# Optimization experiments

Hardware: AMD Instinct MI355X
Metric: run time of the kernel (lower is better)

## Reference

```python
import jax, jax.numpy as jnp
import numpy as np

S = 64   # state_dim
C = 27   # children per internal node


def setup_inputs() -> dict:
    key = jax.random.key(0)
    ks = jax.random.split(key, 16)
    def f(k, shp, scale=0.02):
        return jax.random.normal(k, shp, dtype=jnp.float32) * scale
    return {
        "external_input": f(ks[0], (S, 5), 1.0),
        "state0":  f(ks[1], (S, 5), 0.01),          # root state buffer
        "states1": f(ks[2], (C, S, 5), 0.01),        # 27 level-1 node states
        "states2": f(ks[3], (C, C, S, 5), 0.01),     # 729 leaf states, grouped by parent
        "agg_W0":  f(ks[4], (S * 5, S * 5 * C)),     # root child_aggregator
        "agg_b0":  f(ks[5], (S * 5,)),
        "agg_W1":  f(ks[6], (C, S * 5, S * 5 * C)),  # batched level-1 aggregators
        "agg_b1":  f(ks[7], (C, S * 5)),
        "up_W1_0": f(ks[8], (64, S * 10)),           # root update_net layer 1
        "up_b1_0": f(ks[9], (64,)),
        "up_W2_0": f(ks[10], (S * 5, 64)),           # root update_net layer 2
        "up_b2_0": f(ks[11], (S * 5,)),
        "up_W1_1": f(ks[12], (C, 64, S * 10)),       # batched level-1 update_nets
        "up_b1_1": f(ks[13], (C, 64)),
        "up_W2_1": f(ks[14], (C, S * 5, 64)),
        "up_b2_1": f(ks[15], (C, S * 5)),
    }


def reference(external_input, state0, states1, states2,
              agg_W0, agg_b0, agg_W1, agg_b1,
              up_W1_0, up_b1_0, up_W2_0, up_b2_0,
              up_W1_1, up_b1_1, up_W2_1, up_b2_1):
    # --- level 2 (leaves): forward just returns their state ---
    leaf_flat = states2.reshape(C, C * S * 5)  # per level-1 parent: stacked+flattened children

    # --- level 1: all 27 nodes processed as one batched GEMV ---
    agg1 = jnp.einsum('nij,nj->ni', agg_W1, leaf_flat) + agg_b1        # [27, S*5]
    comb1 = jnp.concatenate([states1.reshape(C, S * 5), agg1], axis=-1)  # [27, S*10]
    h1 = jax.nn.relu(jnp.einsum('nkj,nj->nk', up_W1_1, comb1) + up_b1_1)  # [27, 64]
    upd1 = jnp.einsum('nij,nj->ni', up_W2_1, h1) + up_b2_1             # [27, S*5]
    new_states1 = states1 + upd1.reshape(C, S, 5)

    # --- root: external input added, then aggregate updated children ---
    s0 = state0 + external_input
    agg0 = agg_W0 @ new_states1.reshape(-1) + agg_b0                   # [S*5]
    comb0 = jnp.concatenate([s0.reshape(-1), agg0])                    # [S*10]
    h0 = jax.nn.relu(up_W1_0 @ comb0 + up_b1_0)
    new_state0 = s0 + (up_W2_0 @ h0 + up_b2_0).reshape(S, 5)
    return new_state0
```

## Files before the change

kernel.cpp:

```cpp
#include <hip/hip_runtime.h>
#include <hip/hip_bf16.h>


__device__ __forceinline__ float wave_reduce_sum(float v) {
    v += __shfl_xor(v, 32, 64);
    v += __shfl_xor(v, 16, 64);
    v += __shfl_xor(v, 8, 64);
    v += __shfl_xor(v, 4, 64);
    v += __shfl_xor(v, 2, 64);
    v += __shfl_xor(v, 1, 64);
    return v;
}

__device__ __forceinline__ float fma4s(float4 w, float4 x, float acc) {
    acc = fmaf(w.x, x.x, acc);
    acc = fmaf(w.y, x.y, acc);
    acc = fmaf(w.z, x.z, acc);
    acc = fmaf(w.w, x.w, acc);
    return acc;
}

__device__ __forceinline__ float4 add4(float4 a, float4 b) {
    return make_float4(a.x + b.x, a.y + b.y, a.z + b.z, a.w + b.w);
}

__global__ void __launch_bounds__(256) k1_gemv(
    const float* __restrict__ W,
    const float* __restrict__ x,
    const float* __restrict__ bias,
    float*       __restrict__ y)
{
    const int b    = blockIdx.x;
    const int node = b / 80;
    const int row0 = node * 320 + (b % 80) * 4;
    const int tid  = threadIdx.x;

    const float4* __restrict__ xf  = reinterpret_cast<const float4*>(x) + (size_t)node * 2160;
    const float4* __restrict__ w0p = reinterpret_cast<const float4*>(W) + (size_t)(row0 + 0) * 2160;
    const float4* __restrict__ w1p = reinterpret_cast<const float4*>(W) + (size_t)(row0 + 1) * 2160;
    const float4* __restrict__ w2p = reinterpret_cast<const float4*>(W) + (size_t)(row0 + 2) * 2160;
    const float4* __restrict__ w3p = reinterpret_cast<const float4*>(W) + (size_t)(row0 + 3) * 2160;

    float4 a0 = make_float4(0.f, 0.f, 0.f, 0.f), a1 = a0, a2 = a0, a3 = a0;
    for (int j = tid; j < 2160; j += 256) {
        float4 xv = xf[j];
        float4 w0 = w0p[j];
        float4 w1 = w1p[j];
        float4 w2 = w2p[j];
        float4 w3 = w3p[j];
        a0.x = fmaf(w0.x, xv.x, a0.x); a0.y = fmaf(w0.y, xv.y, a0.y);
        a0.z = fmaf(w0.z, xv.z, a0.z); a0.w = fmaf(w0.w, xv.w, a0.w);
        a1.x = fmaf(w1.x, xv.x, a1.x); a1.y = fmaf(w1.y, xv.y, a1.y);
        a1.z = fmaf(w1.z, xv.z, a1.z); a1.w = fmaf(w1.w, xv.w, a1.w);
        a2.x = fmaf(w2.x, xv.x, a2.x); a2.y = fmaf(w2.y, xv.y, a2.y);
        a2.z = fmaf(w2.z, xv.z, a2.z); a2.w = fmaf(w2.w, xv.w, a2.w);
        a3.x = fmaf(w3.x, xv.x, a3.x); a3.y = fmaf(w3.y, xv.y, a3.y);
        a3.z = fmaf(w3.z, xv.z, a3.z); a3.w = fmaf(w3.w, xv.w, a3.w);
    }
    float s0 = (a0.x + a0.y) + (a0.z + a0.w);
    float s1 = (a1.x + a1.y) + (a1.z + a1.w);
    float s2 = (a2.x + a2.y) + (a2.z + a2.w);
    float s3 = (a3.x + a3.y) + (a3.z + a3.w);
    s0 = wave_reduce_sum(s0);
    s1 = wave_reduce_sum(s1);
    s2 = wave_reduce_sum(s2);
    s3 = wave_reduce_sum(s3);

    __shared__ float red[4][4];
    const int wv = tid >> 6, lane = tid & 63;
    if (lane == 0) { red[wv][0] = s0; red[wv][1] = s1; red[wv][2] = s2; red[wv][3] = s3; }
    __syncthreads();
    if (tid < 4) {
        float v = red[0][tid] + red[1][tid] + red[2][tid] + red[3][tid];
        y[row0 + tid] = v + bias[row0 + tid];
    }
}

__global__ void __launch_bounds__(256) k2a_h(
    const float* __restrict__ states1,
    const float* __restrict__ agg1,
    const float* __restrict__ W1,
    const float* __restrict__ b1,
    float*       __restrict__ h1)
{
    __shared__ float comb[640];
    const int nb  = blockIdx.x;
    const int n   = nb / 16;
    const int tid = threadIdx.x;

    float4* combf = reinterpret_cast<float4*>(comb);
    const float4* __restrict__ s1f = reinterpret_cast<const float4*>(states1) + (size_t)n * 80;
    const float4* __restrict__ a1f = reinterpret_cast<const float4*>(agg1) + (size_t)n * 80;
    if (tid < 80)       combf[tid] = s1f[tid];
    else if (tid < 160) combf[tid] = a1f[tid - 80];
    __syncthreads();

    const int wv = tid >> 6, lane = tid & 63;
    const int k  = (nb % 16) * 4 + wv;
    const float4* __restrict__ Wf = reinterpret_cast<const float4*>(W1) + ((size_t)n * 64 + k) * 160;
    float acc = 0.f;
    #pragma unroll
    for (int j = lane; j < 160; j += 64)
        acc = fma4s(Wf[j], combf[j], acc);
    acc = wave_reduce_sum(acc);
    if (lane == 0) h1[n * 64 + k] = fmaxf(acc + b1[n * 64 + k], 0.f);
}

__global__ void __launch_bounds__(256) k2b_ns(
    const float* __restrict__ states1,
    const float* __restrict__ h1,
    const float* __restrict__ W2,
    const float* __restrict__ b2,
    float*       __restrict__ ns1)
{
    const int tid  = threadIdx.x;
    const int wv   = tid >> 6, lane = tid & 63;
    const int i    = blockIdx.x * 4 + wv;
    const int n    = i / 320;
    float acc = W2[(size_t)i * 64 + lane] * h1[n * 64 + lane];
    acc = wave_reduce_sum(acc);
    if (lane == 0) ns1[i] = states1[i] + acc + b2[i];
}

__global__ void __launch_bounds__(256) k3_gemv(
    const float* __restrict__ W,
    const float* __restrict__ x,
    float*       __restrict__ yp)
{
    const int b   = blockIdx.x;
    const int cs  = b / 80;
    const int r0  = (b % 80) * 4;
    const int tid = threadIdx.x;

    const float4* __restrict__ xf  = reinterpret_cast<const float4*>(x);
    const float4* __restrict__ w0p = reinterpret_cast<const float4*>(W) + (size_t)(r0 + 0) * 2160;
    const float4* __restrict__ w1p = reinterpret_cast<const float4*>(W) + (size_t)(r0 + 1) * 2160;
    const float4* __restrict__ w2p = reinterpret_cast<const float4*>(W) + (size_t)(r0 + 2) * 2160;
    const float4* __restrict__ w3p = reinterpret_cast<const float4*>(W) + (size_t)(r0 + 3) * 2160;

    float4 a0 = make_float4(0.f, 0.f, 0.f, 0.f), a1 = a0, a2 = a0, a3 = a0;
    const int jend = cs * 540 + 540;
    for (int j = cs * 540 + tid; j < jend; j += 256) {
        float4 xv = xf[j];
        float4 w0 = w0p[j];
        float4 w1 = w1p[j];
        float4 w2 = w2p[j];
        float4 w3 = w3p[j];
        a0.x = fmaf(w0.x, xv.x, a0.x); a0.y = fmaf(w0.y, xv.y, a0.y);
        a0.z = fmaf(w0.z, xv.z, a0.z); a0.w = fmaf(w0.w, xv.w, a0.w);
        a1.x = fmaf(w1.x, xv.x, a1.x); a1.y = fmaf(w1.y, xv.y, a1.y);
        a1.z = fmaf(w1.z, xv.z, a1.z); a1.w = fmaf(w1.w, xv.w, a1.w);
        a2.x = fmaf(w2.x, xv.x, a2.x); a2.y = fmaf(w2.y, xv.y, a2.y);
        a2.z = fmaf(w2.z, xv.z, a2.z); a2.w = fmaf(w2.w, xv.w, a2.w);
        a3.x = fmaf(w3.x, xv.x, a3.x); a3.y = fmaf(w3.y, xv.y, a3.y);
        a3.z = fmaf(w3.z, xv.z, a3.z); a3.w = fmaf(w3.w, xv.w, a3.w);
    }
    float s0 = (a0.x + a0.y) + (a0.z + a0.w);
    float s1 = (a1.x + a1.y) + (a1.z + a1.w);
    float s2 = (a2.x + a2.y) + (a2.z + a2.w);
    float s3 = (a3.x + a3.y) + (a3.z + a3.w);
    s0 = wave_reduce_sum(s0);
    s1 = wave_reduce_sum(s1);
    s2 = wave_reduce_sum(s2);
    s3 = wave_reduce_sum(s3);

    __shared__ float red[4][4];
    const int wv = tid >> 6, lane = tid & 63;
    if (lane == 0) { red[wv][0] = s0; red[wv][1] = s1; red[wv][2] = s2; red[wv][3] = s3; }
    __syncthreads();
    if (tid < 4) {
        yp[cs * 320 + r0 + tid] =
            red[0][tid] + red[1][tid] + red[2][tid] + red[3][tid];
    }
}

__global__ void __launch_bounds__(256) K4_root(
    const float* __restrict__ state0,
    const float* __restrict__ ext,
    const float* __restrict__ agg0p,
    const float* __restrict__ aggb0,
    const float* __restrict__ W1,
    const float* __restrict__ b1,
    const float* __restrict__ W2,
    const float* __restrict__ b2,
    float*       __restrict__ out)
{
    __shared__ __align__(16) float comb[640];
    __shared__ float h[64];
    const int tid = threadIdx.x;
    const int wv  = tid >> 6, lane = tid & 63;

    float4* combf = reinterpret_cast<float4*>(comb);
    const float4* __restrict__ s0f = reinterpret_cast<const float4*>(state0);
    const float4* __restrict__ exf = reinterpret_cast<const float4*>(ext);
    const float4* __restrict__ p0  = reinterpret_cast<const float4*>(agg0p);
    const float4* __restrict__ b0f = reinterpret_cast<const float4*>(aggb0);
    if (tid < 80) {
        combf[tid] = add4(s0f[tid], exf[tid]);
    } else if (tid < 160) {
        int jj = tid - 80;
        combf[tid] = add4(add4(add4(p0[jj], p0[80 + jj]), add4(p0[160 + jj], p0[240 + jj])), b0f[jj]);
    }
    __syncthreads();

    const float4* __restrict__ cf = reinterpret_cast<const float4*>(comb);
    for (int kk = 0; kk < 16; ++kk) {
        const int k = wv * 16 + kk;
        const float4* __restrict__ Wf = reinterpret_cast<const float4*>(W1) + (size_t)k * 160;
        float acc = 0.f;
        for (int j = lane; j < 160; j += 64)
            acc = fma4s(Wf[j], cf[j], acc);
        acc = wave_reduce_sum(acc);
        if (lane == 0) h[k] = fmaxf(acc + b1[k], 0.f);
    }
    __syncthreads();

    const int i = blockIdx.x * 4 + wv;
    float acc = W2[(size_t)i * 64 + lane] * h[lane];
    acc = wave_reduce_sum(acc);
    if (lane == 0) out[i] = comb[i] + acc + b2[i];
}

extern "C" void kernel_launch(void* const* d_in, const int* in_sizes, int n_in,
                              void* d_out, int out_size, void* d_ws, size_t ws_size,
                              hipStream_t stream) {
    const float* ext      = (const float*)d_in[0];
    const float* state0   = (const float*)d_in[1];
    const float* states1  = (const float*)d_in[2];
    const float* states2  = (const float*)d_in[3];
    const float* agg_W0   = (const float*)d_in[4];
    const float* agg_b0   = (const float*)d_in[5];
    const float* agg_W1   = (const float*)d_in[6];
    const float* agg_b1   = (const float*)d_in[7];
    const float* up_W1_0  = (const float*)d_in[8];
    const float* up_b1_0  = (const float*)d_in[9];
    const float* up_W2_0  = (const float*)d_in[10];
    const float* up_b2_0  = (const float*)d_in[11];
    const float* up_W1_1  = (const float*)d_in[12];
    const float* up_b1_1  = (const float*)d_in[13];
    const float* up_W2_1  = (const float*)d_in[14];
    const float* up_b2_1  = (const float*)d_in[15];

    float* out   = (float*)d_out;
    float* ws    = (float*)d_ws;
    float* agg1  = ws;
    float* h1    = ws + 8640;
    float* ns1   = ws + 10368;
    float* agg0p = ws + 19008;

    k1_gemv<<<2160, 256, 0, stream>>>(agg_W1, states2, agg_b1, agg1);
    k2a_h  <<<432,  256, 0, stream>>>(states1, agg1, up_W1_1, up_b1_1, h1);
    k2b_ns <<<2160, 256, 0, stream>>>(states1, h1, up_W2_1, up_b2_1, ns1);
    k3_gemv<<<320,  256, 0, stream>>>(agg_W0, ns1, agg0p);
    K4_root<<<80,   256, 0, stream>>>(state0, ext, agg0p, agg_b0,
                                      up_W1_0, up_b1_0, up_W2_0, up_b2_0, out);
}
```

Baseline: 83.29 us.

## Fuse four tail kernels into one launch synchronized by global atomic counters

Merges the h1, new-state, root aggregation and root update stages into a single kernel whose block ranges play each stage role. Dependencies between stages are enforced with per-stage atomic counters that blocks spin on, which removes three kernel launch boundaries and their drain gaps. A memset of the counters is added each call. Spin-waiting relies on producer blocks being scheduled before consumers, and relaxed atomics without fences risk ordering and forward-progress problems. The root aggregation also now reads ns1 as scalar atomic loads rather than float4.

```diff
diff --git a/kernel.cpp b/kernel.cpp
--- a/kernel.cpp
+++ b/kernel.cpp
@@ -1,6 +1,13 @@
 #include <hip/hip_runtime.h>
 #include <hip/hip_bf16.h>
 
+
+__device__ __forceinline__ float ag_load(const float* p) {
+    return __hip_atomic_load(p, __ATOMIC_RELAXED, __HIP_MEMORY_SCOPE_AGENT);
+}
+__device__ __forceinline__ void ag_store(float* p, float v) {
+    __hip_atomic_store(p, v, __ATOMIC_RELAXED, __HIP_MEMORY_SCOPE_AGENT);
+}
 
 __device__ __forceinline__ float wave_reduce_sum(float v) {
     v += __shfl_xor(v, 32, 64);
@@ -22,6 +29,19 @@
 
 __device__ __forceinline__ float4 add4(float4 a, float4 b) {
     return make_float4(a.x + b.x, a.y + b.y, a.z + b.z, a.w + b.w);
+}
+
+__device__ __forceinline__ void wait_cnt(int* c, int target) {
+    if (threadIdx.x == 0) {
+        while (__hip_atomic_load(c, __ATOMIC_RELAXED, __HIP_MEMORY_SCOPE_AGENT) < target)
+            __builtin_amdgcn_s_sleep(2);
+    }
+    __syncthreads();
+}
+__device__ __forceinline__ void bump_cnt(int* c) {
+    __syncthreads();
+    if (threadIdx.x == 0)
+        __hip_atomic_fetch_add(c, 1, __ATOMIC_RELAXED, __HIP_MEMORY_SCOPE_AGENT);
 }
 
 __global__ void __launch_bounds__(256) k1_gemv(
@@ -76,182 +96,157 @@
     }
 }
 
-__global__ void __launch_bounds__(256) k2a_h(
-    const float* __restrict__ states1,
-    const float* __restrict__ agg1,
-    const float* __restrict__ W1,
-    const float* __restrict__ b1,
-    float*       __restrict__ h1)
-{
-    __shared__ float comb[640];
-    const int nb  = blockIdx.x;
-    const int n   = nb / 16;
-    const int tid = threadIdx.x;
-
-    float4* combf = reinterpret_cast<float4*>(comb);
-    const float4* __restrict__ s1f = reinterpret_cast<const float4*>(states1) + (size_t)n * 80;
-    const float4* __restrict__ a1f = reinterpret_cast<const float4*>(agg1) + (size_t)n * 80;
-    if (tid < 80)       combf[tid] = s1f[tid];
-    else if (tid < 160) combf[tid] = a1f[tid - 80];
-    __syncthreads();
-
-    const int wv = tid >> 6, lane = tid & 63;
-    const int k  = (nb % 16) * 4 + wv;
-    const float4* __restrict__ Wf = reinterpret_cast<const float4*>(W1) + ((size_t)n * 64 + k) * 160;
-    float acc = 0.f;
-    #pragma unroll
-    for (int j = lane; j < 160; j += 64)
-        acc = fma4s(Wf[j], combf[j], acc);
-    acc = wave_reduce_sum(acc);
-    if (lane == 0) h1[n * 64 + k] = fmaxf(acc + b1[n * 64 + k], 0.f);
-}
-
-__global__ void __launch_bounds__(256) k2b_ns(
-    const float* __restrict__ states1,
-    const float* __restrict__ h1,
-    const float* __restrict__ W2,
-    const float* __restrict__ b2,
-    float*       __restrict__ ns1)
-{
-    const int tid  = threadIdx.x;
-    const int wv   = tid >> 6, lane = tid & 63;
-    const int i    = blockIdx.x * 4 + wv;
-    const int n    = i / 320;
-    float acc = W2[(size_t)i * 64 + lane] * h1[n * 64 + lane];
-    acc = wave_reduce_sum(acc);
-    if (lane == 0) ns1[i] = states1[i] + acc + b2[i];
-}
-
-__global__ void __launch_bounds__(256) k3_gemv(
-    const float* __restrict__ W,
-    const float* __restrict__ x,
-    float*       __restrict__ yp)
-{
+struct TP {
+    const float *states1, *uW1_1, *ub1_1, *uW2_1, *ub2_1;
+    const float *aggW0, *aggb0;
+    const float *state0, *ext;
+    const float *uW1_0, *ub1_0, *uW2_0, *ub2_0;
+    const float *agg1;
+    float *h1, *ns1, *agg0p, *h0, *out;
+    int *cnt;
+};
+
+__global__ void __launch_bounds__(256, 8) tail_fused(TP p) {
+    __shared__ __align__(16) float sh[640];
+    __shared__ float hsm[64];
     const int b   = blockIdx.x;
-    const int cs  = b / 80;
-    const int r0  = (b % 80) * 4;
-    const int tid = threadIdx.x;
-
-    const float4* __restrict__ xf  = reinterpret_cast<const float4*>(x);
-    const float4* __restrict__ w0p = reinterpret_cast<const float4*>(W) + (size_t)(r0 + 0) * 2160;
-    const float4* __restrict__ w1p = reinterpret_cast<const float4*>(W) + (size_t)(r0 + 1) * 2160;
-    const float4* __restrict__ w2p = reinterpret_cast<const float4*>(W) + (size_t)(r0 + 2) * 2160;
-    const float4* __restrict__ w3p = reinterpret_cast<const float4*>(W) + (size_t)(r0 + 3) * 2160;
-
-    float4 a0 = make_float4(0.f, 0.f, 0.f, 0.f), a1 = a0, a2 = a0, a3 = a0;
-    const int jend = cs * 540 + 540;
-    for (int j = cs * 540 + tid; j < jend; j += 256) {
-        float4 xv = xf[j];
-        float4 w0 = w0p[j];
-        float4 w1 = w1p[j];
-        float4 w2 = w2p[j];
-        float4 w3 = w3p[j];
-        a0.x = fmaf(w0.x, xv.x, a0.x); a0.y = fmaf(w0.y, xv.y, a0.y);
-        a0.z = fmaf(w0.z, xv.z, a0.z); a0.w = fmaf(w0.w, xv.w, a0.w);
-        a1.x = fmaf(w1.x, xv.x, a1.x); a1.y = fmaf(w1.y, xv.y, a1.y);
-        a1.z = fmaf(w1.z, xv.z, a1.z); a1.w = fmaf(w1.w, xv.w, a1.w);
-        a2.x = fmaf(w2.x, xv.x, a2.x); a2.y = fmaf(w2.y, xv.y, a2.y);
-        a2.z = fmaf(w2.z, xv.z, a2.z); a2.w = fmaf(w2.w, xv.w, a2.w);
-        a3.x = fmaf(w3.x, xv.x, a3.x); a3.y = fmaf(w3.y, xv.y, a3.y);
-        a3.z = fmaf(w3.z, xv.z, a3.z); a3.w = fmaf(w3.w, xv.w, a3.w);
-    }
-    float s0 = (a0.x + a0.y) + (a0.z + a0.w);
-    float s1 = (a1.x + a1.y) + (a1.z + a1.w);
-    float s2 = (a2.x + a2.y) + (a2.z + a2.w);
-    float s3 = (a3.x + a3.y) + (a3.z + a3.w);
-    s0 = wave_reduce_sum(s0);
-    s1 = wave_reduce_sum(s1);
-    s2 = wave_reduce_sum(s2);
-    s3 = wave_reduce_sum(s3);
-
-    __shared__ float red[4][4];
-    const int wv = tid >> 6, lane = tid & 63;
-    if (lane == 0) { red[wv][0] = s0; red[wv][1] = s1; red[wv][2] = s2; red[wv][3] = s3; }
-    __syncthreads();
-    if (tid < 4) {
-        yp[cs * 320 + r0 + tid] =
-            red[0][tid] + red[1][tid] + red[2][tid] + red[3][tid];
-    }
-}
-
-__global__ void __launch_bounds__(256) K4_root(
-    const float* __restrict__ state0,
-    const float* __restrict__ ext,
-    const float* __restrict__ agg0p,
-    const float* __restrict__ aggb0,
-    const float* __restrict__ W1,
-    const float* __restrict__ b1,
-    const float* __restrict__ W2,
-    const float* __restrict__ b2,
-    float*       __restrict__ out)
-{
-    __shared__ __align__(16) float comb[640];
-    __shared__ float h[64];
     const int tid = threadIdx.x;
     const int wv  = tid >> 6, lane = tid & 63;
 
-    float4* combf = reinterpret_cast<float4*>(comb);
-    const float4* __restrict__ s0f = reinterpret_cast<const float4*>(state0);
-    const float4* __restrict__ exf = reinterpret_cast<const float4*>(ext);
-    const float4* __restrict__ p0  = reinterpret_cast<const float4*>(agg0p);
-    const float4* __restrict__ b0f = reinterpret_cast<const float4*>(aggb0);
-    if (tid < 80) {
-        combf[tid] = add4(s0f[tid], exf[tid]);
-    } else if (tid < 160) {
-        int jj = tid - 80;
-        combf[tid] = add4(add4(add4(p0[jj], p0[80 + jj]), add4(p0[160 + jj], p0[240 + jj])), b0f[jj]);
-    }
-    __syncthreads();
-
-    const float4* __restrict__ cf = reinterpret_cast<const float4*>(comb);
-    for (int kk = 0; kk < 16; ++kk) {
-        const int k = wv * 16 + kk;
-        const float4* __restrict__ Wf = reinterpret_cast<const float4*>(W1) + (size_t)k * 160;
+    if (b < 432) {
+        const int n = b >> 4;
+        float4* shf = reinterpret_cast<float4*>(sh);
+        const float4* __restrict__ s1f = reinterpret_cast<const float4*>(p.states1) + (size_t)n * 80;
+        const float4* __restrict__ a1f = reinterpret_cast<const float4*>(p.agg1) + (size_t)n * 80;
+        if (tid < 80)       shf[tid] = s1f[tid];
+        else if (tid < 160) shf[tid] = a1f[tid - 80];
+        __syncthreads();
+
+        const int k = (b & 15) * 4 + wv;
+        const float4* __restrict__ Wf = reinterpret_cast<const float4*>(p.uW1_1) + ((size_t)n * 64 + k) * 160;
         float acc = 0.f;
+        #pragma unroll
+        for (int j = lane; j < 160; j += 64)
+            acc = fma4s(Wf[j], shf[j], acc);
+        acc = wave_reduce_sum(acc);
+        if (lane == 0)
+            ag_store(p.h1 + n * 64 + k, fmaxf(acc + p.ub1_1[n * 64 + k], 0.f));
+        bump_cnt(&p.cnt[n]);
+    } else if (b < 972) {
+        const int t = b - 432;
+        const int n = t / 20;
+        wait_cnt(&p.cnt[n], 16);
+        const int base = t * 16;
+        float hv = ag_load(p.h1 + n * 64 + lane);
+        #pragma unroll
+        for (int rr = 0; rr < 4; ++rr) {
+            const int row = base + wv * 4 + rr;
+            float acc = p.uW2_1[(size_t)row * 64 + lane] * hv;
+            acc = wave_reduce_sum(acc);
+            if (lane == 0)
+                ag_store(p.ns1 + row, p.states1[row] + acc + p.ub2_1[row]);
+        }
+        bump_cnt(&p.cnt[27]);
+    } else if (b < 1292) {
+        wait_cnt(&p.cnt[27], 540);
+        const int t  = b - 972;
+        const int cs = t / 80;
+        const int r0 = (t % 80) * 4;
+        const float4* __restrict__ w0p = reinterpret_cast<const float4*>(p.aggW0) + (size_t)(r0 + 0) * 2160;
+        const float4* __restrict__ w1p = reinterpret_cast<const float4*>(p.aggW0) + (size_t)(r0 + 1) * 2160;
+        const float4* __restrict__ w2p = reinterpret_cast<const float4*>(p.aggW0) + (size_t)(r0 + 2) * 2160;
+        const float4* __restrict__ w3p = reinterpret_cast<const float4*>(p.aggW0) + (size_t)(r0 + 3) * 2160;
+
+        float a0 = 0.f, a1 = 0.f, a2 = 0.f, a3 = 0.f;
+        const int jend = cs * 540 + 540;
+        for (int j = cs * 540 + tid; j < jend; j += 256) {
+            float x0 = ag_load(p.ns1 + 4 * j);
+            float x1 = ag_load(p.ns1 + 4 * j + 1);
+            float x2 = ag_load(p.ns1 + 4 * j + 2);
+            float x3 = ag_load(p.ns1 + 4 * j + 3);
+            float4 w0 = w0p[j];
+            float4 w1 = w1p[j];
+            float4 w2 = w2p[j];
+            float4 w3 = w3p[j];
+            a0 = fmaf(w0.x, x0, fmaf(w0.y, x1, fmaf(w0.z, x2, fmaf(w0.w, x3, a0))));
+            a1 = fmaf(w1.x, x0, fmaf(w1.y, x1, fmaf(w1.z, x2, fmaf(w1.w, x3, a1))));
+            a2 = fmaf(w2.x, x0, fmaf(w2.y, x1, fmaf(w2.z, x2, fmaf(w2.w, x3, a2))));
+            a3 = fmaf(w3.x, x0, fmaf(w3.y, x1, fmaf(w3.z, x2, fmaf(w3.w, x3, a3))));
+        }
+        a0 = wave_reduce_sum(a0);
+        a1 = wave_reduce_sum(a1);
+        a2 = wave_reduce_sum(a2);
+        a3 = wave_reduce_sum(a3);
+        if (lane == 0) {
+            hsm[wv * 4 + 0] = a0; hsm[wv * 4 + 1] = a1;
+            hsm[wv * 4 + 2] = a2; hsm[wv * 4 + 3] = a3;
+        }
+        __syncthreads();
+        if (tid < 4) {
+            float v = hsm[tid] + hsm[4 + tid] + hsm[8 + tid] + hsm[12 + tid];
+            ag_store(p.agg0p + cs * 320 + r0 + tid, v);
+        }
+        bump_cnt(&p.cnt[28]);
+    } else if (b < 1308) {
+        wait_cnt(&p.cnt[28], 320);
+        for (int j = tid; j < 320; j += 256) {
+            sh[j]       = p.state0[j] + p.ext[j];
+            sh[320 + j] = ag_load(p.agg0p + j) + ag_load(p.agg0p + 320 + j)
+                        + ag_load(p.agg0p + 640 + j) + ag_load(p.agg0p + 960 + j)
+                        + p.aggb0[j];
+        }
+        __syncthreads();
+        const float4* __restrict__ cf = reinterpret_cast<const float4*>(sh);
+        const int k = (b - 1292) * 4 + wv;
+        const float4* __restrict__ Wf = reinterpret_cast<const float4*>(p.uW1_0) + (size_t)k * 160;
+        float acc = 0.f;
+        #pragma unroll
         for (int j = lane; j < 160; j += 64)
             acc = fma4s(Wf[j], cf[j], acc);
         acc = wave_reduce_sum(acc);
-        if (lane == 0) h[k] = fmaxf(acc + b1[k], 0.f);
-    }
-    __syncthreads();
-
-    const int i = blockIdx.x * 4 + wv;
-    float acc = W2[(size_t)i * 64 + lane] * h[lane];
-    acc = wave_reduce_sum(acc);
-    if (lane == 0) out[i] = comb[i] + acc + b2[i];
+        if (lane == 0)
+            ag_store(p.h0 + k, fmaxf(acc + p.ub1_0[k], 0.f));
+        bump_cnt(&p.cnt[29]);
+    } else {
+        wait_cnt(&p.cnt[29], 16);
+        const int i = (b - 1308) * 4 + wv;
+        float acc = p.uW2_0[(size_t)i * 64 + lane] * ag_load(p.h0 + lane);
+        acc = wave_reduce_sum(acc);
+        if (lane == 0)
+            p.out[i] = p.state0[i] + p.ext[i] + acc + p.ub2_0[i];
+    }
 }
 
 extern "C" void kernel_launch(void* const* d_in, const int* in_sizes, int n_in,
                               void* d_out, int out_size, void* d_ws, size_t ws_size,
                               hipStream_t stream) {
-    const float* ext      = (const float*)d_in[0];
-    const float* state0   = (const float*)d_in[1];
-    const float* states1  = (const float*)d_in[2];
-    const float* states2  = (const float*)d_in[3];
-    const float* agg_W0   = (const float*)d_in[4];
-    const float* agg_b0   = (const float*)d_in[5];
-    const float* agg_W1   = (const float*)d_in[6];
-    const float* agg_b1   = (const float*)d_in[7];
-    const float* up_W1_0  = (const float*)d_in[8];
-    const float* up_b1_0  = (const float*)d_in[9];
-    const float* up_W2_0  = (const float*)d_in[10];
-    const float* up_b2_0  = (const float*)d_in[11];
-    const float* up_W1_1  = (const float*)d_in[12];
-    const float* up_b1_1  = (const float*)d_in[13];
-    const float* up_W2_1  = (const float*)d_in[14];
-    const float* up_b2_1  = (const float*)d_in[15];
-
-    float* out   = (float*)d_out;
-    float* ws    = (float*)d_ws;
-    float* agg1  = ws;
-    float* h1    = ws + 8640;
-    float* ns1   = ws + 10368;
-    float* agg0p = ws + 19008;
-
-    k1_gemv<<<2160, 256, 0, stream>>>(agg_W1, states2, agg_b1, agg1);
-    k2a_h  <<<432,  256, 0, stream>>>(states1, agg1, up_W1_1, up_b1_1, h1);
-    k2b_ns <<<2160, 256, 0, stream>>>(states1, h1, up_W2_1, up_b2_1, ns1);
-    k3_gemv<<<320,  256, 0, stream>>>(agg_W0, ns1, agg0p);
-    K4_root<<<80,   256, 0, stream>>>(state0, ext, agg0p, agg_b0,
-                                      up_W1_0, up_b1_0, up_W2_0, up_b2_0, out);
-}
+    float* ws = (float*)d_ws;
+
+    TP p;
+    p.states1 = (const float*)d_in[2];
+    p.uW1_1   = (const float*)d_in[12];
+    p.ub1_1   = (const float*)d_in[13];
+    p.uW2_1   = (const float*)d_in[14];
+    p.ub2_1   = (const float*)d_in[15];
+    p.aggW0   = (const float*)d_in[4];
+    p.aggb0   = (const float*)d_in[5];
+    p.state0  = (const float*)d_in[1];
+    p.ext     = (const float*)d_in[0];
+    p.uW1_0   = (const float*)d_in[8];
+    p.ub1_0   = (const float*)d_in[9];
+    p.uW2_0   = (const float*)d_in[10];
+    p.ub2_0   = (const float*)d_in[11];
+    p.agg1    = ws;
+    p.h1      = ws + 8640;
+    p.ns1     = ws + 10368;
+    p.agg0p   = ws + 19008;
+    p.h0      = ws + 20288;
+    p.out     = (float*)d_out;
+    p.cnt     = (int*)(ws + 20352);
+
+    hipMemsetAsync(p.cnt, 0, 30 * sizeof(int), stream);
+
+    k1_gemv<<<2160, 256, 0, stream>>>((const float*)d_in[6], (const float*)d_in[3],
+                                      (const float*)d_in[7], (float*)p.agg1);
+    tail_fused<<<1388, 256, 0, stream>>>(p);
+}
```

Measured after the change: 127.2 us. 52.8% more time.
